# Performance work log

Hardware: AMD Instinct MI355X
Metric: run time of the kernel (lower is better)

## Reference

```python
import jax, jax.numpy as jnp
import numpy as np

SUBSTEP = 10
FRAMES = 24
T = FRAMES * SUBSTEP
DT = 1.0 / 60.0 / SUBSTEP
SLOPE_DEG = 20.0
COS_S = float(np.cos(np.deg2rad(SLOPE_DEG)))
SIN_S = float(np.sin(np.deg2rad(SLOPE_DEG)))
INIT_HEIGHT = 0.1
N_VERTS = 2_000_000
GRAVITY = jnp.array([0.0, -9.8, 0.0], dtype=jnp.float32)
CONTACT_N = jnp.array([-SIN_S, COS_S, 0.0], dtype=jnp.float32)
EPS = 1e-6


def quat_mul(a, b):
    w1, x1, y1, z1 = a[0], a[1], a[2], a[3]
    w2, x2, y2, z2 = b[0], b[1], b[2], b[3]
    return jnp.stack([
        w1 * w2 - x1 * x2 - y1 * y2 - z1 * z2,
        w1 * x2 + x1 * w2 + y1 * z2 - z1 * y2,
        w1 * y2 + y1 * w2 + z1 * x2 - x1 * z2,
        w1 * z2 + z1 * w2 + x1 * y2 - y1 * x2,
    ])


def quat_to_matrix(q):
    q = q / jnp.linalg.norm(q)
    w, x, y, z = q[0], q[1], q[2], q[3]
    return jnp.stack([
        jnp.stack([1 - 2 * y * y - 2 * z * z, 2 * x * y - 2 * w * z, 2 * x * z + 2 * w * y]),
        jnp.stack([2 * x * y + 2 * w * z, 1 - 2 * x * x - 2 * z * z, 2 * y * z - 2 * w * x]),
        jnp.stack([2 * x * z - 2 * w * y, 2 * y * z + 2 * w * x, 1 - 2 * x * x - 2 * y * y]),
    ])


def cross_matrix(a):
    z = jnp.zeros((), dtype=a.dtype)
    return jnp.stack([
        jnp.stack([z, -a[2], a[1]]),
        jnp.stack([a[2], z, -a[0]]),
        jnp.stack([-a[1], a[0], z]),
    ])


def setup_inputs() -> dict:
    key = jax.random.key(0)
    k1, k2, k3 = jax.random.split(key, 3)
    return {
        "x": jax.random.normal(k1, (N_VERTS, 3), dtype=jnp.float32) * 0.2,
        "mass_center": jnp.zeros((3,), dtype=jnp.float32),
        "init_trans": jax.random.normal(k2, (3,), dtype=jnp.float32) * 0.3 + jnp.array([0.3, 0.5, 0.0]),
        "init_quat": jnp.ones((4,), dtype=jnp.float32),
        "init_v": jax.random.normal(k3, (3,), dtype=jnp.float32) * 0.1,
        "kn": jnp.array([0.5], dtype=jnp.float32),
        "mu": jnp.array([0.4], dtype=jnp.float32),
        "linear_damping": jnp.array([0.999], dtype=jnp.float32),
        "angular_damping": jnp.array([0.998], dtype=jnp.float32),
    }


def _simulate(x, mass_center, init_trans, init_quat, init_v, kn, mu, linear_damping, angular_damping):
    n = x.shape[0]
    mass = jnp.asarray(float(n), dtype=x.dtype)  # unit mass per vertex
    inv_mass = 1.0 / mass
    r = x - mass_center
    # inertia_reference = sum_i m*( (r.r) I - outer(r,r) )
    inertia = jnp.sum(jnp.einsum('ni,ni->n', r, r)) * jnp.eye(3, dtype=x.dtype) - jnp.einsum('ni,nj->ij', r, r)
    kn0, mu0 = kn[0], mu[0]
    ld, ad = linear_damping[0], angular_damping[0]
    eye3 = jnp.eye(3, dtype=x.dtype)

    def step(carry, _):
        trans, quat, v, omega = carry
        Rm = quat_to_matrix(quat)
        Rx = x @ Rm.T                                   # [N,3]
        xi = trans + Rx + mass_center                   # world positions
        vi_all = v + jnp.cross(omega[None, :], Rx)      # per-vertex velocities
        d = xi @ CONTACT_N
        rel_v = vi_all @ CONTACT_N
        mask = (d < -COS_S * INIT_HEIGHT) & (rel_v < 0.0)
        num = jnp.sum(mask)
        numf = jnp.maximum(num, 1).astype(x.dtype)
        sum_pos = jnp.sum(x * mask[:, None].astype(x.dtype), axis=0)
        ri = sum_pos / numf
        Ri = Rm @ ri
        vi = v + jnp.cross(omega, Ri)
        v_n = jnp.dot(vi, CONTACT_N) * CONTACT_N
        v_t = vi - v_n
        vn_new = -kn0 * v_n
        alpha = jnp.maximum(1.0 - mu0 * (1.0 + kn0) * (jnp.linalg.norm(v_n) / (jnp.linalg.norm(v_t) + EPS)), 0.0)
        vi_new = vn_new + alpha * v_t
        I = Rm @ inertia @ Rm.T
        I_inv = jnp.linalg.inv(I)
        Rri = cross_matrix(Ri)
        kmat = inv_mass * eye3 - Rri @ I_inv @ Rri
        J = jnp.linalg.solve(kmat, vi_new - vi)
        hit = num > 0
        dv = jnp.where(hit, J * inv_mass, 0.0)
        domega = jnp.where(hit, I_inv @ Rri @ J, 0.0)
        v_new = (v + GRAVITY * DT) * ld + dv
        omega_new = omega * ad + domega
        trans_new = trans + DT * v_new
        wq = jnp.concatenate([jnp.zeros((1,), dtype=x.dtype), omega_new]) * (0.5 * DT)
        quat_new = quat + quat_mul(wq, quat)
        quat_new = quat_new / jnp.linalg.norm(quat_new)
        new_carry = (trans_new, quat_new, v_new, omega_new)
        return new_carry, jnp.concatenate([trans_new, quat_new])

    carry0 = (init_trans, init_quat / jnp.linalg.norm(init_quat), init_v, jnp.zeros(3, dtype=x.dtype))
    _, traj = jax.lax.scan(step, carry0, None, length=T)
    return traj  # [T, 7] = translation(3) + quaternion(4) per substep


def reference(x, mass_center, init_trans, init_quat, init_v, kn, mu, linear_damping, angular_damping):
    return _simulate(x, mass_center, init_trans, init_quat, init_v, kn, mu, linear_damping, angular_damping)
```

## Files before the change

kernel.cpp:

```cpp
#include <hip/hip_runtime.h>

#define GRID    256
#define BLOCK   512
#define NWAVES  (BLOCK / 64)
#define CHUNK   7813

typedef unsigned long long u64;

__device__ __forceinline__ u64 rec_load(const u64* p) {
  return __hip_atomic_load(p, __ATOMIC_RELAXED, __HIP_MEMORY_SCOPE_AGENT);
}
__device__ __forceinline__ void rec_store(u64* p, u64 v) {
  __hip_atomic_store(p, v, __ATOMIC_RELAXED, __HIP_MEMORY_SCOPE_AGENT);
}
__device__ __forceinline__ u64 rec_pack(float f, unsigned tag) {
  return (u64)__float_as_uint(f) | ((u64)tag << 32);
}

template <int NV>
__device__ __forceinline__ void block_reduce(float* v, float* sm) {
  #pragma unroll
  for (int off = 32; off > 0; off >>= 1) {
    #pragma unroll
    for (int k = 0; k < NV; ++k) v[k] += __shfl_down(v[k], off, 64);
  }
  const int lane = threadIdx.x & 63;
  const int wid  = threadIdx.x >> 6;
  if (lane == 0) {
    #pragma unroll
    for (int k = 0; k < NV; ++k) sm[wid * NV + k] = v[k];
  }
  __syncthreads();
  if (threadIdx.x == 0) {
    #pragma unroll
    for (int w = 1; w < NWAVES; ++w) {
      #pragma unroll
      for (int k = 0; k < NV; ++k) v[k] += sm[w * NV + k];
    }
  }
  __syncthreads();
}

__device__ __forceinline__ void mat3_mul(const float* A, const float* B, float* C) {
  #pragma unroll
  for (int i = 0; i < 3; ++i)
    #pragma unroll
    for (int j = 0; j < 3; ++j)
      C[i*3+j] = A[i*3+0]*B[0*3+j] + A[i*3+1]*B[1*3+j] + A[i*3+2]*B[2*3+j];
}
__device__ __forceinline__ void mat3_mul_bt(const float* A, const float* B, float* C) {
  #pragma unroll
  for (int i = 0; i < 3; ++i)
    #pragma unroll
    for (int j = 0; j < 3; ++j)
      C[i*3+j] = A[i*3+0]*B[j*3+0] + A[i*3+1]*B[j*3+1] + A[i*3+2]*B[j*3+2];
}
__device__ __forceinline__ void mat3_inv(const float* m, float* inv) {
  float A =  (m[4]*m[8] - m[5]*m[7]);
  float B = -(m[3]*m[8] - m[5]*m[6]);
  float C =  (m[3]*m[7] - m[4]*m[6]);
  float det = m[0]*A + m[1]*B + m[2]*C;
  float id = 1.0f / det;
  inv[0] = A * id;
  inv[1] = -(m[1]*m[8] - m[2]*m[7]) * id;
  inv[2] =  (m[1]*m[5] - m[2]*m[4]) * id;
  inv[3] = B * id;
  inv[4] =  (m[0]*m[8] - m[2]*m[6]) * id;
  inv[5] = -(m[0]*m[5] - m[2]*m[3]) * id;
  inv[6] = C * id;
  inv[7] = -(m[0]*m[7] - m[1]*m[6]) * id;
  inv[8] =  (m[0]*m[4] - m[1]*m[3]) * id;
}

__global__ __launch_bounds__(BLOCK)
void sim_kernel(const float* __restrict__ xg,
                const float* __restrict__ mc_p,
                const float* __restrict__ itr_p,
                const float* __restrict__ iq_p,
                const float* __restrict__ iv_p,
                const float* __restrict__ kn_p,
                const float* __restrict__ mu_p,
                const float* __restrict__ ldp_p,
                const float* __restrict__ adp_p,
                float* __restrict__ out,
                u64* __restrict__ ws,
                int N, int T)
{
  const int tid = threadIdx.x;
  const int bid = blockIdx.x;

  extern __shared__ float dyn[];
  float* sXx = dyn;
  float* sXy = dyn + CHUNK;
  float* sXz = dyn + 2 * CHUNK;
  __shared__ float s_red[NWAVES * 8];
  __shared__ float s_plane[8];

  const float nx  = (float)(-0.3420201433256687);
  const float ny  = (float)( 0.9396926207859084);
  const float DTF = (float)(1.0 / 60.0 / 10.0);
  const float HDT = (float)(0.5 * (1.0 / 60.0 / 10.0));
  const float DTH = (float)(-0.9396926207859084 * 0.1);
  const float GYDT = -9.8f * (float)(1.0 / 60.0 / 10.0);

  const float mc0 = mc_p[0], mc1 = mc_p[1], mc2 = mc_p[2];

  u64* part0 = ws;
  u64* part1 = ws + 4 * GRID;
  u64* st    = ws + 8 * GRID;
  u64* bufI  = ws + 8 * GRID + 128;

  const int vstart = bid * CHUNK;
  int cl = N - vstart; if (cl > CHUNK) cl = CHUNK; if (cl < 0) cl = 0;

  for (int i = tid; i < cl; i += BLOCK) {
    const float* p = xg + (size_t)(vstart + i) * 3;
    sXx[i] = p[0]; sXy[i] = p[1]; sXz[i] = p[2];
  }
  __syncthreads();

  {
    float v6[6] = {0,0,0,0,0,0};
    for (int i = tid; i < cl; i += BLOCK) {
      float r0 = sXx[i] - mc0, r1 = sXy[i] - mc1, r2 = sXz[i] - mc2;
      v6[0] += r0*r0; v6[1] += r1*r1; v6[2] += r2*r2;
      v6[3] += r0*r1; v6[4] += r0*r2; v6[5] += r1*r2;
    }
    block_reduce<6>(v6, s_red);
    if (tid == 0) {
      #pragma unroll
      for (int k = 0; k < 6; ++k) rec_store(bufI + k * GRID + bid, rec_pack(v6[k], 0xC0FFEEu));
    }
  }

  float In[9];
  if (bid == 0) {
    float v6[6] = {0,0,0,0,0,0};
    if (tid < GRID) {
      u64 r[6];
      int f = 0;
      for (;;) {
        #pragma unroll
        for (int k = 0; k < 6; ++k) r[k] = rec_load(bufI + k * GRID + tid);
        bool ok = true;
        #pragma unroll
        for (int k = 0; k < 6; ++k) ok &= ((unsigned)(r[k] >> 32) == 0xC0FFEEu);
        if (ok) break;
        if ((++f & 15) == 0) __builtin_amdgcn_s_sleep(1);
      }
      #pragma unroll
      for (int k = 0; k < 6; ++k) v6[k] = __uint_as_float((unsigned)r[k]);
    }
    block_reduce<6>(v6, s_red);
    float trc = v6[0] + v6[1] + v6[2];
    In[0] = trc - v6[0]; In[4] = trc - v6[1]; In[8] = trc - v6[2];
    In[1] = -v6[3]; In[3] = -v6[3];
    In[2] = -v6[4]; In[6] = -v6[4];
    In[5] = -v6[5]; In[7] = -v6[5];
  }

  float tr0 = itr_p[0], tr1 = itr_p[1], tr2 = itr_p[2];
  float q0 = iq_p[0], q1 = iq_p[1], q2 = iq_p[2], q3 = iq_p[3];
  {
    float n0 = sqrtf(q0*q0 + q1*q1 + q2*q2 + q3*q3);
    q0 /= n0; q1 /= n0; q2 /= n0; q3 /= n0;
  }
  float v0 = iv_p[0], v1 = iv_p[1], v2 = iv_p[2];
  float om0 = 0.f, om1 = 0.f, om2 = 0.f;
  const float knv = kn_p[0], muv = mu_p[0], ldv = ldp_p[0], adv = adp_p[0];
  const float inv_mass = 1.0f / (float)N;

  float Rm[9];
  float Ii[9];

  if (tid == 0) {
    float qn = sqrtf(q0*q0 + q1*q1 + q2*q2 + q3*q3);
    float w = q0/qn, xq = q1/qn, yq = q2/qn, zq = q3/qn;
    Rm[0] = 1.f - 2.f*yq*yq - 2.f*zq*zq; Rm[1] = 2.f*xq*yq - 2.f*w*zq; Rm[2] = 2.f*xq*zq + 2.f*w*yq;
    Rm[3] = 2.f*xq*yq + 2.f*w*zq; Rm[4] = 1.f - 2.f*xq*xq - 2.f*zq*zq; Rm[5] = 2.f*yq*zq - 2.f*w*xq;
    Rm[6] = 2.f*xq*zq - 2.f*w*yq; Rm[7] = 2.f*yq*zq + 2.f*w*xq; Rm[8] = 1.f - 2.f*xq*xq - 2.f*yq*yq;
    float a0 = Rm[0]*nx + Rm[3]*ny;
    float a1 = Rm[1]*nx + Rm[4]*ny;
    float a2 = Rm[2]*nx + Rm[5]*ny;
    float w0 = ny*om2, w1 = -nx*om2, w2 = nx*om1 - ny*om0;
    float b0 = Rm[0]*w0 + Rm[3]*w1 + Rm[6]*w2;
    float b1 = Rm[1]*w0 + Rm[4]*w1 + Rm[7]*w2;
    float b2 = Rm[2]*w0 + Rm[5]*w1 + Rm[8]*w2;
    float ca = DTH - ((tr0 + mc0)*nx + (tr1 + mc1)*ny);
    float cb = -(v0*nx + v1*ny);
    s_plane[0] = a0; s_plane[1] = a1; s_plane[2] = a2;
    s_plane[3] = b0; s_plane[4] = b1; s_plane[5] = b2;
    s_plane[6] = ca; s_plane[7] = cb;
    if (bid == 0) {
      float Tm[9]; mat3_mul(Rm, In, Tm);
      float Iw[9]; mat3_mul_bt(Tm, Rm, Iw);
      mat3_inv(Iw, Ii);
    }
  }
  __syncthreads();

  for (int t = 0; t < T; ++t) {
    const float a0 = s_plane[0], a1 = s_plane[1], a2 = s_plane[2];
    const float b0 = s_plane[3], b1 = s_plane[4], b2 = s_plane[5];
    const float ca = s_plane[6], cb = s_plane[7];

    float acc[4] = {0.f, 0.f, 0.f, 0.f};
    for (int i = tid; i < cl; i += BLOCK) {
      float x0 = sXx[i], x1 = sXy[i], x2 = sXz[i];
      float da = x0*a0 + x1*a1 + x2*a2;
      float db = x0*b0 + x1*b1 + x2*b2;
      if (da < ca && db < cb) { acc[0] += 1.f; acc[1] += x0; acc[2] += x1; acc[3] += x2; }
    }
    block_reduce<4>(acc, s_red);

    const unsigned want = (unsigned)(t + 1);
    u64* pb = (t & 1) ? part1 : part0;
    if (tid == 0) {
      #pragma unroll
      for (int k = 0; k < 4; ++k) rec_store(pb + k * GRID + bid, rec_pack(acc[k], want));
    }

    if (bid == 0) {
      float tot[4] = {0.f, 0.f, 0.f, 0.f};
      if (tid < GRID) {
        u64 r0, r1, r2, r3;
        int f = 0;
        for (;;) {
          r0 = rec_load(pb + 0 * GRID + tid);
          r1 = rec_load(pb + 1 * GRID + tid);
          r2 = rec_load(pb + 2 * GRID + tid);
          r3 = rec_load(pb + 3 * GRID + tid);
          if ((unsigned)(r0 >> 32) == want && (unsigned)(r1 >> 32) == want &&
              (unsigned)(r2 >> 32) == want && (unsigned)(r3 >> 32) == want) break;
          if ((++f & 15) == 0) __builtin_amdgcn_s_sleep(1);
        }
        tot[0] = __uint_as_float((unsigned)r0);
        tot[1] = __uint_as_float((unsigned)r1);
        tot[2] = __uint_as_float((unsigned)r2);
        tot[3] = __uint_as_float((unsigned)r3);
      }
      block_reduce<4>(tot, s_red);

      if (tid == 0) {
        float num = tot[0];
        float numf = fmaxf(num, 1.0f);
        float ri0 = tot[1] / numf, ri1 = tot[2] / numf, ri2 = tot[3] / numf;
        float Ri0 = Rm[0]*ri0 + Rm[1]*ri1 + Rm[2]*ri2;
        float Ri1 = Rm[3]*ri0 + Rm[4]*ri1 + Rm[5]*ri2;
        float Ri2 = Rm[6]*ri0 + Rm[7]*ri1 + Rm[8]*ri2;
        float dv0 = 0.f, dv1 = 0.f, dv2 = 0.f, dm0 = 0.f, dm1 = 0.f, dm2 = 0.f;
        if (num > 0.0f) {
          float vi0 = v0 + om1*Ri2 - om2*Ri1;
          float vi1 = v1 + om2*Ri0 - om0*Ri2;
          float vi2 = v2 + om0*Ri1 - om1*Ri0;
          float vdn = vi0*nx + vi1*ny;
          float vn0 = vdn*nx, vn1 = vdn*ny;
          float vt0 = vi0 - vn0, vt1 = vi1 - vn1, vt2 = vi2;
          float nvn = sqrtf(vn0*vn0 + vn1*vn1);
          float nvt = sqrtf(vt0*vt0 + vt1*vt1 + vt2*vt2);
          float alpha = fmaxf(1.0f - muv*(1.0f + knv)*(nvn/(nvt + 1e-6f)), 0.0f);
          float dvi0 = (-knv*vn0 + alpha*vt0) - vi0;
          float dvi1 = (-knv*vn1 + alpha*vt1) - vi1;
          float dvi2 = (alpha*vt2) - vi2;
          float Cx[9] = {0.f, -Ri2, Ri1,  Ri2, 0.f, -Ri0,  -Ri1, Ri0, 0.f};
          float T2[9]; mat3_mul(Cx, Ii, T2);
          float T3[9]; mat3_mul(T2, Cx, T3);
          float K[9];
          #pragma unroll
          for (int k = 0; k < 9; ++k) K[k] = -T3[k];
          K[0] += inv_mass; K[4] += inv_mass; K[8] += inv_mass;
          float Ki[9]; mat3_inv(K, Ki);
          float J0 = Ki[0]*dvi0 + Ki[1]*dvi1 + Ki[2]*dvi2;
          float J1 = Ki[3]*dvi0 + Ki[4]*dvi1 + Ki[5]*dvi2;
          float J2 = Ki[6]*dvi0 + Ki[7]*dvi1 + Ki[8]*dvi2;
          dv0 = J0*inv_mass; dv1 = J1*inv_mass; dv2 = J2*inv_mass;
          float c0 = -Ri2*J1 + Ri1*J2;
          float c1 =  Ri2*J0 - Ri0*J2;
          float c2 = -Ri1*J0 + Ri0*J1;
          dm0 = Ii[0]*c0 + Ii[1]*c1 + Ii[2]*c2;
          dm1 = Ii[3]*c0 + Ii[4]*c1 + Ii[5]*c2;
          dm2 = Ii[6]*c0 + Ii[7]*c1 + Ii[8]*c2;
        }
        v0 = v0*ldv + dv0;
        v1 = (v1 + GYDT)*ldv + dv1;
        v2 = v2*ldv + dv2;
        om0 = om0*adv + dm0; om1 = om1*adv + dm1; om2 = om2*adv + dm2;
        tr0 = tr0 + DTF*v0; tr1 = tr1 + DTF*v1; tr2 = tr2 + DTF*v2;
        float wx = om0*HDT, wy = om1*HDT, wz = om2*HDT;
        float dq0 = -wx*q1 - wy*q2 - wz*q3;
        float dq1 =  wx*q0 + wy*q3 - wz*q2;
        float dq2 =  wy*q0 + wz*q1 - wx*q3;
        float dq3 =  wz*q0 + wx*q2 - wy*q1;
        q0 += dq0; q1 += dq1; q2 += dq2; q3 += dq3;
        float qn2 = sqrtf(q0*q0 + q1*q1 + q2*q2 + q3*q3);
        q0 /= qn2; q1 /= qn2; q2 /= qn2; q3 /= qn2;
        float* o = out + (size_t)t * 7;
        o[0] = tr0; o[1] = tr1; o[2] = tr2;
        o[3] = q0;  o[4] = q1;  o[5] = q2;  o[6] = q3;
        float qn = sqrtf(q0*q0 + q1*q1 + q2*q2 + q3*q3);
        float w = q0/qn, xq = q1/qn, yq = q2/qn, zq = q3/qn;
        Rm[0] = 1.f - 2.f*yq*yq - 2.f*zq*zq; Rm[1] = 2.f*xq*yq - 2.f*w*zq; Rm[2] = 2.f*xq*zq + 2.f*w*yq;
        Rm[3] = 2.f*xq*yq + 2.f*w*zq; Rm[4] = 1.f - 2.f*xq*xq - 2.f*zq*zq; Rm[5] = 2.f*yq*zq - 2.f*w*xq;
        Rm[6] = 2.f*xq*zq - 2.f*w*yq; Rm[7] = 2.f*yq*zq + 2.f*w*xq; Rm[8] = 1.f - 2.f*xq*xq - 2.f*yq*yq;
        float na0 = Rm[0]*nx + Rm[3]*ny;
        float na1 = Rm[1]*nx + Rm[4]*ny;
        float na2 = Rm[2]*nx + Rm[5]*ny;
        float w0 = ny*om2, w1 = -nx*om2, w2 = nx*om1 - ny*om0;
        float nb0 = Rm[0]*w0 + Rm[3]*w1 + Rm[6]*w2;
        float nb1 = Rm[1]*w0 + Rm[4]*w1 + Rm[7]*w2;
        float nb2 = Rm[2]*w0 + Rm[5]*w1 + Rm[8]*w2;
        float nca = DTH - ((tr0 + mc0)*nx + (tr1 + mc1)*ny);
        float ncb = -(v0*nx + v1*ny);
        s_plane[0] = na0; s_plane[1] = na1; s_plane[2] = na2;
        s_plane[3] = nb0; s_plane[4] = nb1; s_plane[5] = nb2;
        s_plane[6] = nca; s_plane[7] = ncb;
      }
      __syncthreads();
      if (tid < 64) {
        u64* sl = st + (size_t)((t + 1) & 1) * 64;
        rec_store(sl + tid, rec_pack(s_plane[tid & 7], want));
      }
      if (tid == 0) {
        float Tm[9]; mat3_mul(Rm, In, Tm);
        float Iw[9]; mat3_mul_bt(Tm, Rm, Iw);
        mat3_inv(Iw, Ii);
      }
    } else {
      if (tid < 8) {
        const u64* sl = st + (size_t)((t + 1) & 1) * 64 + (size_t)(bid & 7) * 8;
        u64 r; int f = 0;
        for (;;) {
          r = rec_load(sl + tid);
          if ((unsigned)(r >> 32) == want) break;
          if ((++f & 31) == 0) __builtin_amdgcn_s_sleep(1);
        }
        s_plane[tid] = __uint_as_float((unsigned)r);
      }
      __syncthreads();
    }
  }
}

extern "C" void kernel_launch(void* const* d_in, const int* in_sizes, int n_in,
                              void* d_out, int out_size, void* d_ws, size_t ws_size,
                              hipStream_t stream) {
  const float* x   = (const float*)d_in[0];
  const float* mc  = (const float*)d_in[1];
  const float* itr = (const float*)d_in[2];
  const float* iq  = (const float*)d_in[3];
  const float* iv  = (const float*)d_in[4];
  const float* kn  = (const float*)d_in[5];
  const float* mu  = (const float*)d_in[6];
  const float* ldp = (const float*)d_in[7];
  const float* adp = (const float*)d_in[8];
  float* out = (float*)d_out;
  u64* ws  = (u64*)d_ws;
  int N = in_sizes[0] / 3;
  int T = out_size / 7;

  const int dyn_lds = 3 * CHUNK * 4;
  hipFuncSetAttribute((const void*)sim_kernel,
                      hipFuncAttributeMaxDynamicSharedMemorySize, dyn_lds);

  void* args[] = {(void*)&x, (void*)&mc, (void*)&itr, (void*)&iq, (void*)&iv,
                  (void*)&kn, (void*)&mu, (void*)&ldp, (void*)&adp,
                  (void*)&out, (void*)&ws, (void*)&N, (void*)&T};
  hipLaunchCooperativeKernel((void*)sim_kernel, dim3(GRID), dim3(BLOCK),
                             args, dyn_lds, stream);
}
```

Before: 1.424 ms.

## Speculatively batch multiple substeps per grid sync assuming no contact

Each block now assumes no contact occurs and evaluates up to KMAX future substeps' contact predicates in a single pass over its shared-memory vertices, so several substeps share one cross-block reduction and sync. Block 0 walks the predicted trajectory until the first contact, applies the impulse there, and broadcasts the corrected state together with how many steps were consumed. After a contact the next round runs one step at a time. When angular velocity is zero, a cheaper single-plane test is used. The intent is to amortize the per-substep global sync latency, at the cost of more ALU work per vertex, more registers and wasted speculation whenever contact happens early in a batch.

```diff
diff --git a/kernel.cpp b/kernel.cpp
--- a/kernel.cpp
+++ b/kernel.cpp
@@ -4,6 +4,7 @@
 #define BLOCK   512
 #define NWAVES  (BLOCK / 64)
 #define CHUNK   7813
+#define KMAX    8
 
 typedef unsigned long long u64;
 
@@ -93,8 +94,12 @@
   float* sXx = dyn;
   float* sXy = dyn + CHUNK;
   float* sXz = dyn + 2 * CHUNK;
-  __shared__ float s_red[NWAVES * 8];
-  __shared__ float s_plane[8];
+  __shared__ float s_red[NWAVES * 4 * KMAX];
+  __shared__ float s_planes[KMAX][8];
+  __shared__ float s_traj[KMAX + 1][13];
+  __shared__ float s_tot[4 * KMAX];
+  __shared__ float s_state[16];
+  __shared__ int   s_mode;
 
   const float nx  = (float)(-0.3420201433256687);
   const float ny  = (float)( 0.9396926207859084);
@@ -105,10 +110,9 @@
 
   const float mc0 = mc_p[0], mc1 = mc_p[1], mc2 = mc_p[2];
 
-  u64* part0 = ws;
-  u64* part1 = ws + 4 * GRID;
-  u64* st    = ws + 8 * GRID;
-  u64* bufI  = ws + 8 * GRID + 128;
+  u64* part = ws;
+  u64* st   = ws + 2 * GRID * 32;
+  u64* bufI = ws + 2 * GRID * 32 + 128;
 
   const int vstart = bid * CHUNK;
   int cl = N - vstart; if (cl > CHUNK) cl = CHUNK; if (cl < 0) cl = 0;
@@ -170,173 +174,320 @@
   const float knv = kn_p[0], muv = mu_p[0], ldv = ldp_p[0], adv = adp_p[0];
   const float inv_mass = 1.0f / (float)N;
 
-  float Rm[9];
-  float Ii[9];
-
-  if (tid == 0) {
-    float qn = sqrtf(q0*q0 + q1*q1 + q2*q2 + q3*q3);
-    float w = q0/qn, xq = q1/qn, yq = q2/qn, zq = q3/qn;
-    Rm[0] = 1.f - 2.f*yq*yq - 2.f*zq*zq; Rm[1] = 2.f*xq*yq - 2.f*w*zq; Rm[2] = 2.f*xq*zq + 2.f*w*yq;
-    Rm[3] = 2.f*xq*yq + 2.f*w*zq; Rm[4] = 1.f - 2.f*xq*xq - 2.f*zq*zq; Rm[5] = 2.f*yq*zq - 2.f*w*xq;
-    Rm[6] = 2.f*xq*zq - 2.f*w*yq; Rm[7] = 2.f*yq*zq + 2.f*w*xq; Rm[8] = 1.f - 2.f*xq*xq - 2.f*yq*yq;
-    float a0 = Rm[0]*nx + Rm[3]*ny;
-    float a1 = Rm[1]*nx + Rm[4]*ny;
-    float a2 = Rm[2]*nx + Rm[5]*ny;
-    float w0 = ny*om2, w1 = -nx*om2, w2 = nx*om1 - ny*om0;
-    float b0 = Rm[0]*w0 + Rm[3]*w1 + Rm[6]*w2;
-    float b1 = Rm[1]*w0 + Rm[4]*w1 + Rm[7]*w2;
-    float b2 = Rm[2]*w0 + Rm[5]*w1 + Rm[8]*w2;
-    float ca = DTH - ((tr0 + mc0)*nx + (tr1 + mc1)*ny);
-    float cb = -(v0*nx + v1*ny);
-    s_plane[0] = a0; s_plane[1] = a1; s_plane[2] = a2;
-    s_plane[3] = b0; s_plane[4] = b1; s_plane[5] = b2;
-    s_plane[6] = ca; s_plane[7] = cb;
+  int t_base = 0;
+  int rnd = 0;
+  int Ksched = KMAX;
+
+  while (t_base < T) {
+    const int rem = T - t_base;
+    const int Kr = (Ksched < rem) ? Ksched : rem;
+    const unsigned want = (unsigned)(rnd + 1);
+
+    if (tid == 0) {
+      int mode1 = (om0 == 0.f && om1 == 0.f && om2 == 0.f) ? 1 : 0;
+      s_mode = mode1;
+      #pragma unroll
+      for (int k = 0; k < KMAX; ++k) {
+        if (k < Kr) {
+          s_traj[k][0] = tr0; s_traj[k][1] = tr1; s_traj[k][2] = tr2;
+          s_traj[k][3] = q0;  s_traj[k][4] = q1;  s_traj[k][5] = q2;  s_traj[k][6] = q3;
+          s_traj[k][7] = v0;  s_traj[k][8] = v1;  s_traj[k][9] = v2;
+          s_traj[k][10] = om0; s_traj[k][11] = om1; s_traj[k][12] = om2;
+          float qn = sqrtf(q0*q0 + q1*q1 + q2*q2 + q3*q3);
+          float w = q0/qn, xq = q1/qn, yq = q2/qn, zq = q3/qn;
+          float R0 = 1.f - 2.f*yq*yq - 2.f*zq*zq, R1 = 2.f*xq*yq - 2.f*w*zq, R2 = 2.f*xq*zq + 2.f*w*yq;
+          float R3 = 2.f*xq*yq + 2.f*w*zq, R4 = 1.f - 2.f*xq*xq - 2.f*zq*zq, R5 = 2.f*yq*zq - 2.f*w*xq;
+          float R6 = 2.f*xq*zq - 2.f*w*yq, R7 = 2.f*yq*zq + 2.f*w*xq, R8 = 1.f - 2.f*xq*xq - 2.f*yq*yq;
+          float a0 = R0*nx + R3*ny;
+          float a1 = R1*nx + R4*ny;
+          float a2 = R2*nx + R5*ny;
+          float w0 = ny*om2, w1 = -nx*om2, w2 = nx*om1 - ny*om0;
+          float b0 = R0*w0 + R3*w1 + R6*w2;
+          float b1 = R1*w0 + R4*w1 + R7*w2;
+          float b2 = R2*w0 + R5*w1 + R8*w2;
+          float ca = DTH - ((tr0 + mc0)*nx + (tr1 + mc1)*ny);
+          float cb = -(v0*nx + v1*ny);
+          if (mode1) {
+            if (cb > 0.f) {
+              s_planes[k][0] = a0; s_planes[k][1] = a1; s_planes[k][2] = a2; s_planes[k][3] = ca;
+            } else {
+              s_planes[k][0] = 0.f; s_planes[k][1] = 0.f; s_planes[k][2] = 0.f; s_planes[k][3] = -1e30f;
+            }
+          } else {
+            s_planes[k][0] = a0; s_planes[k][1] = a1; s_planes[k][2] = a2; s_planes[k][3] = ca;
+            s_planes[k][4] = b0; s_planes[k][5] = b1; s_planes[k][6] = b2; s_planes[k][7] = cb;
+          }
+          v0 = v0*ldv; v1 = (v1 + GYDT)*ldv; v2 = v2*ldv;
+          om0 = om0*adv; om1 = om1*adv; om2 = om2*adv;
+          tr0 += DTF*v0; tr1 += DTF*v1; tr2 += DTF*v2;
+          float wx = om0*HDT, wy = om1*HDT, wz = om2*HDT;
+          float dq0 = -wx*q1 - wy*q2 - wz*q3;
+          float dq1 =  wx*q0 + wy*q3 - wz*q2;
+          float dq2 =  wy*q0 + wz*q1 - wx*q3;
+          float dq3 =  wz*q0 + wx*q2 - wy*q1;
+          q0 += dq0; q1 += dq1; q2 += dq2; q3 += dq3;
+          float qn2 = sqrtf(q0*q0 + q1*q1 + q2*q2 + q3*q3);
+          q0 /= qn2; q1 /= qn2; q2 /= qn2; q3 /= qn2;
+        } else {
+          s_planes[k][0] = 0.f; s_planes[k][1] = 0.f; s_planes[k][2] = 0.f; s_planes[k][3] = -1e30f;
+          s_planes[k][4] = 0.f; s_planes[k][5] = 0.f; s_planes[k][6] = 0.f; s_planes[k][7] = -1e30f;
+        }
+      }
+      s_traj[Kr][0] = tr0; s_traj[Kr][1] = tr1; s_traj[Kr][2] = tr2;
+      s_traj[Kr][3] = q0;  s_traj[Kr][4] = q1;  s_traj[Kr][5] = q2;  s_traj[Kr][6] = q3;
+      s_traj[Kr][7] = v0;  s_traj[Kr][8] = v1;  s_traj[Kr][9] = v2;
+      s_traj[Kr][10] = om0; s_traj[Kr][11] = om1; s_traj[Kr][12] = om2;
+    }
+    __syncthreads();
+
+    float accf[4 * KMAX];
+    #pragma unroll
+    for (int w = 0; w < 4 * KMAX; ++w) accf[w] = 0.f;
+
+    if (s_mode) {
+      float pa0[KMAX], pa1[KMAX], pa2[KMAX], pca[KMAX];
+      #pragma unroll
+      for (int k = 0; k < KMAX; ++k) {
+        pa0[k] = s_planes[k][0]; pa1[k] = s_planes[k][1];
+        pa2[k] = s_planes[k][2]; pca[k] = s_planes[k][3];
+      }
+      for (int i = tid; i < cl; i += BLOCK) {
+        float x0 = sXx[i], x1 = sXy[i], x2 = sXz[i];
+        #pragma unroll
+        for (int k = 0; k < KMAX; ++k) {
+          float da = x0*pa0[k] + x1*pa1[k] + x2*pa2[k];
+          float sel = (da < pca[k]) ? 1.f : 0.f;
+          accf[k*4+0] += sel;
+          accf[k*4+1] = fmaf(sel, x0, accf[k*4+1]);
+          accf[k*4+2] = fmaf(sel, x1, accf[k*4+2]);
+          accf[k*4+3] = fmaf(sel, x2, accf[k*4+3]);
+        }
+      }
+    } else {
+      float pa0[KMAX], pa1[KMAX], pa2[KMAX], pca[KMAX];
+      float pb0[KMAX], pb1[KMAX], pb2[KMAX], pcb[KMAX];
+      #pragma unroll
+      for (int k = 0; k < KMAX; ++k) {
+        pa0[k] = s_planes[k][0]; pa1[k] = s_planes[k][1];
+        pa2[k] = s_planes[k][2]; pca[k] = s_planes[k][3];
+        pb0[k] = s_planes[k][4]; pb1[k] = s_planes[k][5];
+        pb2[k] = s_planes[k][6]; pcb[k] = s_planes[k][7];
+      }
+      for (int i = tid; i < cl; i += BLOCK) {
+        float x0 = sXx[i], x1 = sXy[i], x2 = sXz[i];
+        #pragma unroll
+        for (int k = 0; k < KMAX; ++k) {
+          float da = x0*pa0[k] + x1*pa1[k] + x2*pa2[k];
+          float db = x0*pb0[k] + x1*pb1[k] + x2*pb2[k];
+          float sel = (da < pca[k] && db < pcb[k]) ? 1.f : 0.f;
+          accf[k*4+0] += sel;
+          accf[k*4+1] = fmaf(sel, x0, accf[k*4+1]);
+          accf[k*4+2] = fmaf(sel, x1, accf[k*4+2]);
+          accf[k*4+3] = fmaf(sel, x2, accf[k*4+3]);
+        }
+      }
+    }
+
+    #pragma unroll
+    for (int off = 32; off > 0; off >>= 1) {
+      #pragma unroll
+      for (int w = 0; w < 4 * KMAX; ++w) accf[w] += __shfl_down(accf[w], off, 64);
+    }
+    {
+      const int lane = tid & 63, wid = tid >> 6;
+      if (lane == 0) {
+        #pragma unroll
+        for (int w = 0; w < 4 * KMAX; ++w) s_red[wid * 32 + w] = accf[w];
+      }
+    }
+    __syncthreads();
+    {
+      u64* pb = part + (size_t)(rnd & 1) * GRID * 32 + (size_t)bid * 32;
+      if (tid < 32) {
+        float tw = s_red[tid];
+        #pragma unroll
+        for (int ww = 1; ww < NWAVES; ++ww) tw += s_red[ww * 32 + tid];
+        rec_store(pb + tid, rec_pack(tw, want));
+      }
+    }
+
     if (bid == 0) {
-      float Tm[9]; mat3_mul(Rm, In, Tm);
-      float Iw[9]; mat3_mul_bt(Tm, Rm, Iw);
-      mat3_inv(Iw, Ii);
-    }
-  }
-  __syncthreads();
-
-  for (int t = 0; t < T; ++t) {
-    const float a0 = s_plane[0], a1 = s_plane[1], a2 = s_plane[2];
-    const float b0 = s_plane[3], b1 = s_plane[4], b2 = s_plane[5];
-    const float ca = s_plane[6], cb = s_plane[7];
-
-    float acc[4] = {0.f, 0.f, 0.f, 0.f};
-    for (int i = tid; i < cl; i += BLOCK) {
-      float x0 = sXx[i], x1 = sXy[i], x2 = sXz[i];
-      float da = x0*a0 + x1*a1 + x2*a2;
-      float db = x0*b0 + x1*b1 + x2*b2;
-      if (da < ca && db < cb) { acc[0] += 1.f; acc[1] += x0; acc[2] += x1; acc[3] += x2; }
-    }
-    block_reduce<4>(acc, s_red);
-
-    const unsigned want = (unsigned)(t + 1);
-    u64* pb = (t & 1) ? part1 : part0;
-    if (tid == 0) {
-      #pragma unroll
-      for (int k = 0; k < 4; ++k) rec_store(pb + k * GRID + bid, rec_pack(acc[k], want));
-    }
-
-    if (bid == 0) {
-      float tot[4] = {0.f, 0.f, 0.f, 0.f};
-      if (tid < GRID) {
-        u64 r0, r1, r2, r3;
+      __syncthreads();
+
+      float tot[4 * KMAX];
+      #pragma unroll
+      for (int w = 0; w < 4 * KMAX; ++w) tot[w] = 0.f;
+      {
+        const u64* pp = part + (size_t)(rnd & 1) * GRID * 32
+                             + (size_t)(tid >> 1) * 32 + (size_t)(tid & 1) * 16;
+        u64 r[16];
         int f = 0;
         for (;;) {
-          r0 = rec_load(pb + 0 * GRID + tid);
-          r1 = rec_load(pb + 1 * GRID + tid);
-          r2 = rec_load(pb + 2 * GRID + tid);
-          r3 = rec_load(pb + 3 * GRID + tid);
-          if ((unsigned)(r0 >> 32) == want && (unsigned)(r1 >> 32) == want &&
-              (unsigned)(r2 >> 32) == want && (unsigned)(r3 >> 32) == want) break;
+          #pragma unroll
+          for (int w = 0; w < 16; ++w) r[w] = rec_load(pp + w);
+          bool ok = true;
+          #pragma unroll
+          for (int w = 0; w < 16; ++w) ok &= ((unsigned)(r[w] >> 32) == want);
+          if (ok) break;
           if ((++f & 15) == 0) __builtin_amdgcn_s_sleep(1);
         }
-        tot[0] = __uint_as_float((unsigned)r0);
-        tot[1] = __uint_as_float((unsigned)r1);
-        tot[2] = __uint_as_float((unsigned)r2);
-        tot[3] = __uint_as_float((unsigned)r3);
-      }
-      block_reduce<4>(tot, s_red);
+        if ((tid & 1) == 0) {
+          #pragma unroll
+          for (int w = 0; w < 16; ++w) tot[w] = __uint_as_float((unsigned)r[w]);
+        } else {
+          #pragma unroll
+          for (int w = 0; w < 16; ++w) tot[16 + w] = __uint_as_float((unsigned)r[w]);
+        }
+      }
+      #pragma unroll
+      for (int off = 32; off > 0; off >>= 1) {
+        #pragma unroll
+        for (int w = 0; w < 4 * KMAX; ++w) tot[w] += __shfl_down(tot[w], off, 64);
+      }
+      {
+        const int lane = tid & 63, wid = tid >> 6;
+        if (lane == 0) {
+          #pragma unroll
+          for (int w = 0; w < 4 * KMAX; ++w) s_red[wid * 32 + w] = tot[w];
+        }
+      }
+      __syncthreads();
+      if (tid < 32) {
+        float tw = s_red[tid];
+        #pragma unroll
+        for (int ww = 1; ww < NWAVES; ++ww) tw += s_red[ww * 32 + tid];
+        s_tot[tid] = tw;
+      }
+      __syncthreads();
 
       if (tid == 0) {
-        float num = tot[0];
-        float numf = fmaxf(num, 1.0f);
-        float ri0 = tot[1] / numf, ri1 = tot[2] / numf, ri2 = tot[3] / numf;
-        float Ri0 = Rm[0]*ri0 + Rm[1]*ri1 + Rm[2]*ri2;
-        float Ri1 = Rm[3]*ri0 + Rm[4]*ri1 + Rm[5]*ri2;
-        float Ri2 = Rm[6]*ri0 + Rm[7]*ri1 + Rm[8]*ri2;
-        float dv0 = 0.f, dv1 = 0.f, dv2 = 0.f, dm0 = 0.f, dm1 = 0.f, dm2 = 0.f;
-        if (num > 0.0f) {
-          float vi0 = v0 + om1*Ri2 - om2*Ri1;
-          float vi1 = v1 + om2*Ri0 - om0*Ri2;
-          float vi2 = v2 + om0*Ri1 - om1*Ri0;
-          float vdn = vi0*nx + vi1*ny;
-          float vn0 = vdn*nx, vn1 = vdn*ny;
-          float vt0 = vi0 - vn0, vt1 = vi1 - vn1, vt2 = vi2;
-          float nvn = sqrtf(vn0*vn0 + vn1*vn1);
-          float nvt = sqrtf(vt0*vt0 + vt1*vt1 + vt2*vt2);
-          float alpha = fmaxf(1.0f - muv*(1.0f + knv)*(nvn/(nvt + 1e-6f)), 0.0f);
-          float dvi0 = (-knv*vn0 + alpha*vt0) - vi0;
-          float dvi1 = (-knv*vn1 + alpha*vt1) - vi1;
-          float dvi2 = (alpha*vt2) - vi2;
-          float Cx[9] = {0.f, -Ri2, Ri1,  Ri2, 0.f, -Ri0,  -Ri1, Ri0, 0.f};
-          float T2[9]; mat3_mul(Cx, Ii, T2);
-          float T3[9]; mat3_mul(T2, Cx, T3);
-          float K[9];
-          #pragma unroll
-          for (int k = 0; k < 9; ++k) K[k] = -T3[k];
-          K[0] += inv_mass; K[4] += inv_mass; K[8] += inv_mass;
-          float Ki[9]; mat3_inv(K, Ki);
-          float J0 = Ki[0]*dvi0 + Ki[1]*dvi1 + Ki[2]*dvi2;
-          float J1 = Ki[3]*dvi0 + Ki[4]*dvi1 + Ki[5]*dvi2;
-          float J2 = Ki[6]*dvi0 + Ki[7]*dvi1 + Ki[8]*dvi2;
-          dv0 = J0*inv_mass; dv1 = J1*inv_mass; dv2 = J2*inv_mass;
-          float c0 = -Ri2*J1 + Ri1*J2;
-          float c1 =  Ri2*J0 - Ri0*J2;
-          float c2 = -Ri1*J0 + Ri0*J1;
-          dm0 = Ii[0]*c0 + Ii[1]*c1 + Ii[2]*c2;
-          dm1 = Ii[3]*c0 + Ii[4]*c1 + Ii[5]*c2;
-          dm2 = Ii[6]*c0 + Ii[7]*c1 + Ii[8]*c2;
-        }
-        v0 = v0*ldv + dv0;
-        v1 = (v1 + GYDT)*ldv + dv1;
-        v2 = v2*ldv + dv2;
-        om0 = om0*adv + dm0; om1 = om1*adv + dm1; om2 = om2*adv + dm2;
-        tr0 = tr0 + DTF*v0; tr1 = tr1 + DTF*v1; tr2 = tr2 + DTF*v2;
-        float wx = om0*HDT, wy = om1*HDT, wz = om2*HDT;
-        float dq0 = -wx*q1 - wy*q2 - wz*q3;
-        float dq1 =  wx*q0 + wy*q3 - wz*q2;
-        float dq2 =  wy*q0 + wz*q1 - wx*q3;
-        float dq3 =  wz*q0 + wx*q2 - wy*q1;
-        q0 += dq0; q1 += dq1; q2 += dq2; q3 += dq3;
-        float qn2 = sqrtf(q0*q0 + q1*q1 + q2*q2 + q3*q3);
-        q0 /= qn2; q1 /= qn2; q2 /= qn2; q3 /= qn2;
-        float* o = out + (size_t)t * 7;
-        o[0] = tr0; o[1] = tr1; o[2] = tr2;
-        o[3] = q0;  o[4] = q1;  o[5] = q2;  o[6] = q3;
-        float qn = sqrtf(q0*q0 + q1*q1 + q2*q2 + q3*q3);
-        float w = q0/qn, xq = q1/qn, yq = q2/qn, zq = q3/qn;
-        Rm[0] = 1.f - 2.f*yq*yq - 2.f*zq*zq; Rm[1] = 2.f*xq*yq - 2.f*w*zq; Rm[2] = 2.f*xq*zq + 2.f*w*yq;
-        Rm[3] = 2.f*xq*yq + 2.f*w*zq; Rm[4] = 1.f - 2.f*xq*xq - 2.f*zq*zq; Rm[5] = 2.f*yq*zq - 2.f*w*xq;
-        Rm[6] = 2.f*xq*zq - 2.f*w*yq; Rm[7] = 2.f*yq*zq + 2.f*w*xq; Rm[8] = 1.f - 2.f*xq*xq - 2.f*yq*yq;
-        float na0 = Rm[0]*nx + Rm[3]*ny;
-        float na1 = Rm[1]*nx + Rm[4]*ny;
-        float na2 = Rm[2]*nx + Rm[5]*ny;
-        float w0 = ny*om2, w1 = -nx*om2, w2 = nx*om1 - ny*om0;
-        float nb0 = Rm[0]*w0 + Rm[3]*w1 + Rm[6]*w2;
-        float nb1 = Rm[1]*w0 + Rm[4]*w1 + Rm[7]*w2;
-        float nb2 = Rm[2]*w0 + Rm[5]*w1 + Rm[8]*w2;
-        float nca = DTH - ((tr0 + mc0)*nx + (tr1 + mc1)*ny);
-        float ncb = -(v0*nx + v1*ny);
-        s_plane[0] = na0; s_plane[1] = na1; s_plane[2] = na2;
-        s_plane[3] = nb0; s_plane[4] = nb1; s_plane[5] = nb2;
-        s_plane[6] = nca; s_plane[7] = ncb;
+        int consumed = Kr;
+        unsigned contact = 0;
+        float f0=0,f1=0,f2=0,f3=0,f4=0,f5=0,f6=0,f7=0,f8=0,f9=0,f10=0,f11=0,f12=0;
+        #pragma unroll
+        for (int k = 0; k < KMAX; ++k) {
+          if (k < Kr && !contact) {
+            float num = s_tot[4*k+0];
+            if (num > 0.0f) {
+              float btr0=s_traj[k][0], btr1=s_traj[k][1], btr2=s_traj[k][2];
+              float bq0=s_traj[k][3], bq1=s_traj[k][4], bq2=s_traj[k][5], bq3=s_traj[k][6];
+              float bv0=s_traj[k][7], bv1=s_traj[k][8], bv2=s_traj[k][9];
+              float bo0=s_traj[k][10], bo1=s_traj[k][11], bo2=s_traj[k][12];
+              float qn = sqrtf(bq0*bq0 + bq1*bq1 + bq2*bq2 + bq3*bq3);
+              float w = bq0/qn, xq = bq1/qn, yq = bq2/qn, zq = bq3/qn;
+              float Rm[9];
+              Rm[0] = 1.f - 2.f*yq*yq - 2.f*zq*zq; Rm[1] = 2.f*xq*yq - 2.f*w*zq; Rm[2] = 2.f*xq*zq + 2.f*w*yq;
+              Rm[3] = 2.f*xq*yq + 2.f*w*zq; Rm[4] = 1.f - 2.f*xq*xq - 2.f*zq*zq; Rm[5] = 2.f*yq*zq - 2.f*w*xq;
+              Rm[6] = 2.f*xq*zq - 2.f*w*yq; Rm[7] = 2.f*yq*zq + 2.f*w*xq; Rm[8] = 1.f - 2.f*xq*xq - 2.f*yq*yq;
+              float Tm[9]; mat3_mul(Rm, In, Tm);
+              float Iw[9]; mat3_mul_bt(Tm, Rm, Iw);
+              float Ii[9]; mat3_inv(Iw, Ii);
+              float numf = fmaxf(num, 1.0f);
+              float ri0 = s_tot[4*k+1]/numf, ri1 = s_tot[4*k+2]/numf, ri2 = s_tot[4*k+3]/numf;
+              float Ri0 = Rm[0]*ri0 + Rm[1]*ri1 + Rm[2]*ri2;
+              float Ri1 = Rm[3]*ri0 + Rm[4]*ri1 + Rm[5]*ri2;
+              float Ri2 = Rm[6]*ri0 + Rm[7]*ri1 + Rm[8]*ri2;
+              float vi0 = bv0 + bo1*Ri2 - bo2*Ri1;
+              float vi1 = bv1 + bo2*Ri0 - bo0*Ri2;
+              float vi2 = bv2 + bo0*Ri1 - bo1*Ri0;
+              float vdn = vi0*nx + vi1*ny;
+              float vn0 = vdn*nx, vn1 = vdn*ny;
+              float vt0 = vi0 - vn0, vt1 = vi1 - vn1, vt2 = vi2;
+              float nvn = sqrtf(vn0*vn0 + vn1*vn1);
+              float nvt = sqrtf(vt0*vt0 + vt1*vt1 + vt2*vt2);
+              float alpha = fmaxf(1.0f - muv*(1.0f + knv)*(nvn/(nvt + 1e-6f)), 0.0f);
+              float dvi0 = (-knv*vn0 + alpha*vt0) - vi0;
+              float dvi1 = (-knv*vn1 + alpha*vt1) - vi1;
+              float dvi2 = (alpha*vt2) - vi2;
+              float Cx[9] = {0.f, -Ri2, Ri1,  Ri2, 0.f, -Ri0,  -Ri1, Ri0, 0.f};
+              float T2[9]; mat3_mul(Cx, Ii, T2);
+              float T3[9]; mat3_mul(T2, Cx, T3);
+              float Km[9];
+              #pragma unroll
+              for (int m = 0; m < 9; ++m) Km[m] = -T3[m];
+              Km[0] += inv_mass; Km[4] += inv_mass; Km[8] += inv_mass;
+              float Ki[9]; mat3_inv(Km, Ki);
+              float J0 = Ki[0]*dvi0 + Ki[1]*dvi1 + Ki[2]*dvi2;
+              float J1 = Ki[3]*dvi0 + Ki[4]*dvi1 + Ki[5]*dvi2;
+              float J2 = Ki[6]*dvi0 + Ki[7]*dvi1 + Ki[8]*dvi2;
+              float dv0 = J0*inv_mass, dv1 = J1*inv_mass, dv2 = J2*inv_mass;
+              float c0 = -Ri2*J1 + Ri1*J2;
+              float c1 =  Ri2*J0 - Ri0*J2;
+              float c2 = -Ri1*J0 + Ri0*J1;
+              float dm0 = Ii[0]*c0 + Ii[1]*c1 + Ii[2]*c2;
+              float dm1 = Ii[3]*c0 + Ii[4]*c1 + Ii[5]*c2;
+              float dm2 = Ii[6]*c0 + Ii[7]*c1 + Ii[8]*c2;
+              bv0 = bv0*ldv + dv0;
+              bv1 = (bv1 + GYDT)*ldv + dv1;
+              bv2 = bv2*ldv + dv2;
+              bo0 = bo0*adv + dm0; bo1 = bo1*adv + dm1; bo2 = bo2*adv + dm2;
+              btr0 += DTF*bv0; btr1 += DTF*bv1; btr2 += DTF*bv2;
+              float wx = bo0*HDT, wy = bo1*HDT, wz = bo2*HDT;
+              float dq0 = -wx*bq1 - wy*bq2 - wz*bq3;
+              float dq1 =  wx*bq0 + wy*bq3 - wz*bq2;
+              float dq2 =  wy*bq0 + wz*bq1 - wx*bq3;
+              float dq3 =  wz*bq0 + wx*bq2 - wy*bq1;
+              bq0 += dq0; bq1 += dq1; bq2 += dq2; bq3 += dq3;
+              float qn2 = sqrtf(bq0*bq0 + bq1*bq1 + bq2*bq2 + bq3*bq3);
+              bq0 /= qn2; bq1 /= qn2; bq2 /= qn2; bq3 /= qn2;
+              float* o = out + (size_t)(t_base + k) * 7;
+              o[0] = btr0; o[1] = btr1; o[2] = btr2;
+              o[3] = bq0;  o[4] = bq1;  o[5] = bq2;  o[6] = bq3;
+              f0=btr0; f1=btr1; f2=btr2; f3=bq0; f4=bq1; f5=bq2; f6=bq3;
+              f7=bv0; f8=bv1; f9=bv2; f10=bo0; f11=bo1; f12=bo2;
+              consumed = k + 1; contact = 1;
+            } else {
+              float* o = out + (size_t)(t_base + k) * 7;
+              #pragma unroll
+              for (int j = 0; j < 7; ++j) o[j] = s_traj[k+1][j];
+            }
+          }
+        }
+        if (!contact) {
+          f0=s_traj[Kr][0]; f1=s_traj[Kr][1]; f2=s_traj[Kr][2];
+          f3=s_traj[Kr][3]; f4=s_traj[Kr][4]; f5=s_traj[Kr][5]; f6=s_traj[Kr][6];
+          f7=s_traj[Kr][7]; f8=s_traj[Kr][8]; f9=s_traj[Kr][9];
+          f10=s_traj[Kr][10]; f11=s_traj[Kr][11]; f12=s_traj[Kr][12];
+        }
+        s_state[0]=f0; s_state[1]=f1; s_state[2]=f2;
+        s_state[3]=f3; s_state[4]=f4; s_state[5]=f5; s_state[6]=f6;
+        s_state[7]=f7; s_state[8]=f8; s_state[9]=f9;
+        s_state[10]=f10; s_state[11]=f11; s_state[12]=f12;
+        s_state[13] = __uint_as_float((unsigned)consumed | (contact << 8));
+        s_state[14] = 0.f; s_state[15] = 0.f;
       }
       __syncthreads();
       if (tid < 64) {
-        u64* sl = st + (size_t)((t + 1) & 1) * 64;
-        rec_store(sl + tid, rec_pack(s_plane[tid & 7], want));
-      }
-      if (tid == 0) {
-        float Tm[9]; mat3_mul(Rm, In, Tm);
-        float Iw[9]; mat3_mul_bt(Tm, Rm, Iw);
-        mat3_inv(Iw, Ii);
+        u64* sl = st + (size_t)(rnd & 1) * 64;
+        rec_store(sl + tid, rec_pack(s_state[tid & 15], want));
       }
     } else {
-      if (tid < 8) {
-        const u64* sl = st + (size_t)((t + 1) & 1) * 64 + (size_t)(bid & 7) * 8;
+      if (tid < 16) {
+        const u64* sl = st + (size_t)(rnd & 1) * 64 + (size_t)(bid & 3) * 16;
         u64 r; int f = 0;
         for (;;) {
           r = rec_load(sl + tid);
           if ((unsigned)(r >> 32) == want) break;
           if ((++f & 31) == 0) __builtin_amdgcn_s_sleep(1);
         }
-        s_plane[tid] = __uint_as_float((unsigned)r);
+        s_state[tid] = __uint_as_float((unsigned)r);
       }
       __syncthreads();
+    }
+
+    {
+      unsigned meta = __float_as_uint(s_state[13]);
+      int consumed = (int)(meta & 0xFFu);
+      int contact  = (int)((meta >> 8) & 1u);
+      if (tid == 0) {
+        tr0 = s_state[0]; tr1 = s_state[1]; tr2 = s_state[2];
+        q0 = s_state[3]; q1 = s_state[4]; q2 = s_state[5]; q3 = s_state[6];
+        v0 = s_state[7]; v1 = s_state[8]; v2 = s_state[9];
+        om0 = s_state[10]; om1 = s_state[11]; om2 = s_state[12];
+      }
+      t_base += consumed;
+      Ksched = contact ? 1 : KMAX;
+      ++rnd;
     }
   }
 }
```

Result: slower. 4.666 ms (+227.6%).
